# Kernel tuning notes

Measured on AMD Instinct MI355X. Metric: run time of the kernel, lower is better.

Reference implementation:

```python
import jax, jax.numpy as jnp
import numpy as np

B, S, C, P, M, H = 64, 512, 862, 96, 512, 128  # batch, seq_len, enc_in, pred_len, mem_num, hid_size


def setup_inputs() -> dict:
    key = jax.random.key(0)
    ks = jax.random.split(key, 8)
    x = jax.random.normal(ks[0], (B, S, C), dtype=jnp.float32)
    # nn.Linear default init scale ~ 1/sqrt(fan_in)
    W1 = jax.random.normal(ks[1], (H, S), dtype=jnp.float32) / np.float32(np.sqrt(S))
    b1 = jnp.zeros((H,), dtype=jnp.float32)
    Wp = jax.random.normal(ks[2], (H, H), dtype=jnp.float32) / np.float32(np.sqrt(H))
    bp = jnp.zeros((H,), dtype=jnp.float32)
    W2 = jax.random.normal(ks[3], (P, 2 * H), dtype=jnp.float32) / np.float32(np.sqrt(2 * H))
    b2 = jnp.zeros((P,), dtype=jnp.float32)
    # xavier_normal_ with relu gain: std = sqrt(2) * sqrt(2/(fan_in+fan_out))
    mem_std = np.float32(np.sqrt(2.0) * np.sqrt(2.0 / (M + H)))
    memory = jax.random.normal(ks[4], (M, H), dtype=jnp.float32) * mem_std
    return dict(x=x, W1=W1, b1=b1, Wp=Wp, bp=bp, W2=W2, b2=b2, memory=memory)


def reference(x, W1, b1, Wp, bp, W2, b2, memory):
    b, s, c = x.shape
    # get_repre: Linear1 over seq dim, sigmoid, projector
    r = jax.nn.sigmoid(jnp.einsum('bsc,hs->bch', x, W1) + b1)   # [B, C, H]
    r = jnp.einsum('bch,gh->bcg', r, Wp) + bp                    # [B, C, H]
    r = r.reshape(-1, H)                                         # [N, H], N = B*C
    # memory_enhance: codebook attention (topk/distance loss does not affect output)
    att = jax.nn.softmax(jnp.einsum('nd,fd->nf', r, memory), axis=1)  # [N, M]
    out = jnp.einsum('nf,fd->nd', att, memory)                        # [N, H]
    rep = jnp.concatenate([out, r], axis=1).reshape(b, c, 2 * H)      # [B, C, 2H]
    # predict: Linear2 then permute to [B, pred_len, C]
    res = jnp.einsum('bcd,pd->bcp', rep, W2) + b2
    return jnp.transpose(res, (0, 2, 1))
```

## Files before the change

### kernel.cpp

```cpp
#include <hip/hip_runtime.h>
#include <hip/hip_bf16.h>

typedef __attribute__((ext_vector_type(4))) float f32x4;
typedef __attribute__((ext_vector_type(8))) short s16x8;

#define DEVI __device__ __forceinline__

constexpr int S = 512, C = 862, P = 96, H = 128, BATCH = 64;

DEVI short f2bf(float f) {
  unsigned u = __builtin_bit_cast(unsigned, f);
  u += 0x7fffu + ((u >> 16) & 1u);
  return (short)(u >> 16);
}

DEVI unsigned pk2(float a, float b) {
  return (unsigned)(unsigned short)f2bf(a) | ((unsigned)(unsigned short)f2bf(b) << 16);
}

DEVI s16x8 mk8(const float* v) {
  s16x8 r;
#pragma unroll
  for (int i = 0; i < 8; ++i) r[i] = f2bf(v[i]);
  return r;
}

DEVI void gload16(const void* g, void* l) {
  __builtin_amdgcn_global_load_lds(
      (const __attribute__((address_space(1))) void*)g,
      (__attribute__((address_space(3))) void*)l, 16, 0, 0);
}

template <int NK>
DEVI void redistN(const unsigned* p01, const unsigned* p23, int sA, int hi,
                  s16x8* f) {
#pragma unroll
  for (int kc = 0; kc < NK; ++kc) {
    unsigned a0 = __shfl(p01[2 * kc], sA),      b0 = __shfl(p01[2 * kc + 1], sA);
    unsigned a1 = __shfl(p23[2 * kc], sA),      b1 = __shfl(p23[2 * kc + 1], sA);
    unsigned a2 = __shfl(p01[2 * kc], sA + 16), b2 = __shfl(p01[2 * kc + 1], sA + 16);
    unsigned a3 = __shfl(p23[2 * kc], sA + 16), b3 = __shfl(p23[2 * kc + 1], sA + 16);
    union { s16x8 v; unsigned u[4]; } t;
    t.u[0] = hi ? b0 : a0;
    t.u[1] = hi ? b1 : a1;
    t.u[2] = hi ? b2 : a2;
    t.u[3] = hi ? b3 : a3;
    f[kc] = t.v;
  }
}

__global__ __launch_bounds__(256) void k0_convert(
    const float* __restrict__ W1, const float* __restrict__ Wp,
    const float* __restrict__ W2, const float* __restrict__ mem,
    short* __restrict__ W1b, short* __restrict__ WpS, short* __restrict__ W2b,
    short* __restrict__ membS, short* __restrict__ memTS) {
  int i = blockIdx.x * 256 + threadIdx.x;
  if (i < 65536) { W1b[i] = f2bf(W1[i]); return; }
  i -= 65536;
  if (i < 16384) {
    int g = i >> 7, h = i & 127;
    WpS[(g << 7) + (h ^ ((g & 7) << 3))] = f2bf(Wp[i]);
    return;
  }
  i -= 16384;
  if (i < 24576) { W2b[i] = f2bf(W2[i]); return; }
  i -= 24576;
  if (i < 65536) {
    int f = i >> 7, d = i & 127;
    short v = f2bf(mem[i]);
    membS[((f >> 6) << 13) + ((f & 63) << 7) + (d ^ ((f & 7) << 3))] = v;
    memTS[((f >> 6) << 13) + (d << 6) + ((f & 63) ^ ((d & 7) << 3))] = v;
  }
}

__global__ __launch_bounds__(512, 2) void k12_fused(
    const float* __restrict__ x, const short* __restrict__ W1b,
    const float* __restrict__ b1, const short* __restrict__ WpS,
    const float* __restrict__ bp, const short* __restrict__ membS,
    const short* __restrict__ memTS, const short* __restrict__ W2b,
    const float* __restrict__ b2, float* __restrict__ out) {
  __shared__ __align__(16) char lds[49664];
  float* resf = (float*)lds;

  const int b = blockIdx.y, c0 = blockIdx.x * 128;
  const int valid = (C - c0 < 128) ? (C - c0) : 128;
  const int tid = threadIdx.x, l = tid & 63, w = tid >> 6;
  const int l15 = l & 15, l4 = l >> 4;
  const int sA = l15 + 32 * (l4 & 1);
  const int hi = (l4 >> 1) & 1;
  const int xr = (l15 & 7) << 4;
  const int cb = l4 * 16;
  const int rloc = 16 * w + l15;

  s16x8 rb[4];
  {
    short* xt = (short*)lds;
    short* w1t = (short*)(lds + 16384);
    const int cme = tid & 127, o2 = tid >> 7;
    const bool cv = (c0 + cme) < C;
    const float* xsrc0 = x + (size_t)b * S * C + c0 + cme;
    const int hh = tid >> 2, qq = tid & 3;

    f32x4 acc[8];
#pragma unroll
    for (int t = 0; t < 8; ++t) acc[t] = (f32x4){0.f, 0.f, 0.f, 0.f};

    float xv[2][8];
    s16x8 wv[2];
    {
#pragma unroll
      for (int j = 0; j < 2; ++j) {
        const float* src = xsrc0 + (size_t)((o2 + j * 4) * 8) * C;
#pragma unroll
        for (int i = 0; i < 8; ++i) xv[j][i] = cv ? src[(size_t)i * C] : 0.f;
      }
      const short* wsrc = W1b + hh * 512;
      wv[0] = *(const s16x8*)&wsrc[qq * 8];
      wv[1] = *(const s16x8*)&wsrc[(qq + 4) * 8];
    }

    for (int kt = 0; kt < 8; ++kt) {
#pragma unroll
      for (int j = 0; j < 2; ++j)
        *(s16x8*)&xt[cme * 64 + ((o2 + j * 4) ^ (cme & 7)) * 8] = mk8(xv[j]);
      *(s16x8*)&w1t[hh * 64 + (qq ^ (hh & 7)) * 8] = wv[0];
      *(s16x8*)&w1t[hh * 64 + ((qq + 4) ^ (hh & 7)) * 8] = wv[1];
      if (kt < 7) {
        int kn = kt + 1;
#pragma unroll
        for (int j = 0; j < 2; ++j) {
          const float* src = xsrc0 + (size_t)(kn * 64 + (o2 + j * 4) * 8) * C;
#pragma unroll
          for (int i = 0; i < 8; ++i) xv[j][i] = cv ? src[(size_t)i * C] : 0.f;
        }
        const short* wsrc = W1b + hh * 512 + kn * 64;
        wv[0] = *(const s16x8*)&wsrc[qq * 8];
        wv[1] = *(const s16x8*)&wsrc[(qq + 4) * 8];
      }
      __syncthreads();
      s16x8 bx[2];
#pragma unroll
      for (int kc = 0; kc < 2; ++kc)
        bx[kc] = *(const s16x8*)&xt[rloc * 64 + ((kc * 4 + l4) ^ (l15 & 7)) * 8];
#pragma unroll
      for (int t = 0; t < 8; ++t) {
#pragma unroll
        for (int kc = 0; kc < 2; ++kc) {
          s16x8 af = *(const s16x8*)&w1t[(t * 16 + l15) * 64 + ((kc * 4 + l4) ^ (l15 & 7)) * 8];
          acc[t] = __builtin_amdgcn_mfma_f32_16x16x32_bf16(af, bx[kc], acc[t], 0, 0, 0);
        }
      }
      __syncthreads();
    }

    {
      const char* gwp = (const char*)WpS;
      const char* gmb = (const char*)membS;
#pragma unroll
      for (int i = 0; i < 4; ++i) {
        int o = (w * 4 + i) * 1024;
        gload16(gwp + o + l * 16, lds + 16384 + o);
      }
#pragma unroll
      for (int i = 0; i < 2; ++i) {
        int o = (w * 2 + i) * 1024;
        gload16(gmb + o + l * 16, lds + o);
      }
    }

    unsigned p01[8], p23[8];
#pragma unroll
    for (int t = 0; t < 8; ++t) {
      f32x4 bq = *(const f32x4*)&b1[t * 16 + l4 * 4];
      float s0 = 1.f / (1.f + __expf(-(acc[t][0] + bq[0])));
      float s1 = 1.f / (1.f + __expf(-(acc[t][1] + bq[1])));
      float s2 = 1.f / (1.f + __expf(-(acc[t][2] + bq[2])));
      float s3 = 1.f / (1.f + __expf(-(acc[t][3] + bq[3])));
      p01[t] = pk2(s0, s1);
      p23[t] = pk2(s2, s3);
    }
    redistN<4>(p01, p23, sA, hi, rb);
  }
  __syncthreads();

  unsigned rpk01[8], rpk23[8];
  {
    const char* bufWp = lds + 16384;
#pragma unroll
    for (int gt = 0; gt < 8; ++gt) {
      f32x4 acc = (f32x4){0.f, 0.f, 0.f, 0.f};
#pragma unroll
      for (int kc = 0; kc < 4; ++kc) {
        s16x8 af = *(const s16x8*)(bufWp + (gt * 16 + l15) * 256 + ((kc * 64 + cb) ^ xr));
        acc = __builtin_amdgcn_mfma_f32_16x16x32_bf16(af, rb[kc], acc, 0, 0, 0);
      }
      f32x4 bq = *(const f32x4*)&bp[gt * 16 + l4 * 4];
      rpk01[gt] = pk2(acc[0] + bq[0], acc[1] + bq[1]);
      rpk23[gt] = pk2(acc[2] + bq[2], acc[3] + bq[3]);
    }
  }
  s16x8 r2f[4];
  redistN<4>(rpk01, rpk23, sA, hi, r2f);

  float m_run = -1e30f, s_run = 0.f;
  f32x4 oacc[8];
#pragma unroll
  for (int dt = 0; dt < 8; ++dt) oacc[dt] = (f32x4){0.f, 0.f, 0.f, 0.f};

  for (int s5 = 0; s5 < 8; ++s5) {
    __syncthreads();
    {
      const char* gmt = (const char*)memTS + (size_t)s5 * 16384;
#pragma unroll
      for (int i = 0; i < 2; ++i) {
        int o = (w * 2 + i) * 1024;
        gload16(gmt + o + l * 16, lds + 32768 + o);
      }
    }
    if (s5 < 7) {
      const char* gmb = (const char*)membS + (size_t)(s5 + 1) * 16384;
#pragma unroll
      for (int i = 0; i < 2; ++i) {
        int o = (w * 2 + i) * 1024;
        gload16(gmb + o + l * 16, lds + (((s5 + 1) & 1) << 14) + o);
      }
    }
    f32x4 lg[4];
    {
      const char* bmb = lds + ((s5 & 1) << 14);
#pragma unroll
      for (int ft = 0; ft < 4; ++ft) {
        lg[ft] = (f32x4){0.f, 0.f, 0.f, 0.f};
#pragma unroll
        for (int kc = 0; kc < 4; ++kc) {
          s16x8 af = *(const s16x8*)(bmb + (ft * 16 + l15) * 256 + ((kc * 64 + cb) ^ xr));
          lg[ft] = __builtin_amdgcn_mfma_f32_16x16x32_bf16(af, r2f[kc], lg[ft], 0, 0, 0);
        }
      }
    }
    s16x8 pf[2];
    {
      float mx = lg[0][0];
#pragma unroll
      for (int ft = 0; ft < 4; ++ft)
#pragma unroll
        for (int e = 0; e < 4; ++e) mx = fmaxf(mx, lg[ft][e]);
      mx = fmaxf(mx, __shfl_xor(mx, 16));
      mx = fmaxf(mx, __shfl_xor(mx, 32));
      if (s5 == 0) {
        m_run = mx;
      } else if (!__all(mx <= m_run + 8.f)) {
        float mn = fmaxf(m_run, mx);
        float sc = __expf(m_run - mn);
        s_run *= sc;
        m_run = mn;
#pragma unroll
        for (int dt = 0; dt < 8; ++dt)
#pragma unroll
          for (int e = 0; e < 4; ++e) oacc[dt][e] *= sc;
      }
      float ps = 0.f;
      unsigned ppk01[4], ppk23[4];
#pragma unroll
      for (int ft = 0; ft < 4; ++ft) {
#pragma unroll
        for (int e = 0; e < 4; ++e) {
          float p = __expf(lg[ft][e] - m_run);
          lg[ft][e] = p;
          ps += p;
        }
        ppk01[ft] = pk2(lg[ft][0], lg[ft][1]);
        ppk23[ft] = pk2(lg[ft][2], lg[ft][3]);
      }
      ps += __shfl_xor(ps, 16);
      ps += __shfl_xor(ps, 32);
      s_run += ps;
      redistN<2>(ppk01, ppk23, sA, hi, pf);
    }
    __syncthreads();
    {
      const char* bmt = lds + 32768;
#pragma unroll
      for (int dt = 0; dt < 8; ++dt) {
#pragma unroll
        for (int kc = 0; kc < 2; ++kc) {
          s16x8 af = *(const s16x8*)(bmt + (dt * 16 + l15) * 128 + ((kc * 64 + cb) ^ xr));
          oacc[dt] = __builtin_amdgcn_mfma_f32_16x16x32_bf16(af, pf[kc], oacc[dt], 0, 0, 0);
        }
      }
    }
  }
  __syncthreads();

  s16x8 of[4];
  {
    float inv = 1.f / s_run;
    unsigned opk01[8], opk23[8];
#pragma unroll
    for (int dt = 0; dt < 8; ++dt) {
      opk01[dt] = pk2(oacc[dt][0] * inv, oacc[dt][1] * inv);
      opk23[dt] = pk2(oacc[dt][2] * inv, oacc[dt][3] * inv);
    }
    redistN<4>(opk01, opk23, sA, hi, of);
  }

#pragma unroll
  for (int pt = 0; pt < 6; ++pt) {
    f32x4 acc = (f32x4){0.f, 0.f, 0.f, 0.f};
#pragma unroll
    for (int kc = 0; kc < 4; ++kc) {
      s16x8 af = *(const s16x8*)&W2b[(pt * 16 + l15) * 256 + kc * 32 + l4 * 8];
      acc = __builtin_amdgcn_mfma_f32_16x16x32_bf16(af, of[kc], acc, 0, 0, 0);
    }
#pragma unroll
    for (int kc = 0; kc < 4; ++kc) {
      s16x8 af = *(const s16x8*)&W2b[(pt * 16 + l15) * 256 + 128 + kc * 32 + l4 * 8];
      acc = __builtin_amdgcn_mfma_f32_16x16x32_bf16(af, r2f[kc], acc, 0, 0, 0);
    }
    f32x4 bq = *(const f32x4*)&b2[pt * 16 + l4 * 4];
#pragma unroll
    for (int e = 0; e < 4; ++e)
      resf[rloc * 97 + pt * 16 + l4 * 4 + e] = acc[e] + bq[e];
  }
  __syncthreads();
  {
    int c = tid & 127, p0 = tid >> 7;
    if (c < valid) {
      float* dst = out + (size_t)b * P * C + c0 + c;
#pragma unroll
      for (int j = 0; j < 24; ++j) {
        int p = p0 + j * 4;
        dst[(size_t)p * C] = resf[c * 97 + p];
      }
    }
  }
}

extern "C" void kernel_launch(void* const* d_in, const int* in_sizes, int n_in,
                              void* d_out, int out_size, void* d_ws, size_t ws_size,
                              hipStream_t stream) {
  const float* x   = (const float*)d_in[0];
  const float* W1  = (const float*)d_in[1];
  const float* b1  = (const float*)d_in[2];
  const float* Wp  = (const float*)d_in[3];
  const float* bpv = (const float*)d_in[4];
  const float* W2  = (const float*)d_in[5];
  const float* b2  = (const float*)d_in[6];
  const float* mem = (const float*)d_in[7];
  char* ws = (char*)d_ws;
  short* W1b   = (short*)(ws);
  short* WpS   = (short*)(ws + 131072);
  short* W2b   = (short*)(ws + 163840);
  short* membS = (short*)(ws + 212992);
  short* memTS = (short*)(ws + 344064);
  float* outp = (float*)d_out;

  k0_convert<<<672, 256, 0, stream>>>(W1, Wp, W2, mem, W1b, WpS, W2b, membS, memTS);
  dim3 grid(7, BATCH);
  k12_fused<<<grid, 512, 0, stream>>>(x, W1b, b1, WpS, bpv, membS, memTS, W2b, b2, outp);
}
```

Before: 82.33 us.

## Double block to 1024 threads, split memory attention across two warp groups with merge

The fused kernel now launches 1024 threads per block and divides the work into two groups of 8 waves. In stage 1 the two groups split the H output tiles of the W1 GEMM and exchange the sigmoid results through LDS. In the attention stage each group handles half of the 512 codebook entries with its own online softmax, and the two partial results are merged through LDS using the running max and sum. The change aims to raise parallelism and latency hiding per block. In exchange it adds more LDS (64KB), extra barriers, a bf16-rounded merge of partial outputs, and leaves half the waves idle during the final W2 projection. Launch bounds of (1024,2) with 64KB LDS may also limit occupancy or register budget.

```diff
diff --git a/kernel.cpp b/kernel.cpp
--- a/kernel.cpp
+++ b/kernel.cpp
@@ -17,6 +17,9 @@
 DEVI unsigned pk2(float a, float b) {
   return (unsigned)(unsigned short)f2bf(a) | ((unsigned)(unsigned short)f2bf(b) << 16);
 }
+
+DEVI float bflo(unsigned u) { return __builtin_bit_cast(float, u << 16); }
+DEVI float bfhi(unsigned u) { return __builtin_bit_cast(float, u & 0xffff0000u); }
 
 DEVI s16x8 mk8(const float* v) {
   s16x8 r;
@@ -68,74 +71,68 @@
   if (i < 65536) {
     int f = i >> 7, d = i & 127;
     short v = f2bf(mem[i]);
-    membS[((f >> 6) << 13) + ((f & 63) << 7) + (d ^ ((f & 7) << 3))] = v;
-    memTS[((f >> 6) << 13) + (d << 6) + ((f & 63) ^ ((d & 7) << 3))] = v;
-  }
-}
-
-__global__ __launch_bounds__(512, 2) void k12_fused(
+    membS[((f >> 5) << 12) + ((f & 31) << 7) + (d ^ ((f & 7) << 3))] = v;
+    int fo = (f >> 3) & 3, sw = (d ^ (d >> 2)) & 3;
+    memTS[((f >> 5) << 12) + (d << 5) + ((fo ^ sw) << 3) + (f & 7)] = v;
+  }
+}
+
+__global__ __launch_bounds__(1024, 2) void k12_fused(
     const float* __restrict__ x, const short* __restrict__ W1b,
     const float* __restrict__ b1, const short* __restrict__ WpS,
     const float* __restrict__ bp, const short* __restrict__ membS,
     const short* __restrict__ memTS, const short* __restrict__ W2b,
     const float* __restrict__ b2, float* __restrict__ out) {
-  __shared__ __align__(16) char lds[49664];
+  __shared__ __align__(16) char lds[65536];
   float* resf = (float*)lds;
 
   const int b = blockIdx.y, c0 = blockIdx.x * 128;
   const int valid = (C - c0 < 128) ? (C - c0) : 128;
   const int tid = threadIdx.x, l = tid & 63, w = tid >> 6;
+  const int g = w >> 3, wl = w & 7;
   const int l15 = l & 15, l4 = l >> 4;
   const int sA = l15 + 32 * (l4 & 1);
   const int hi = (l4 >> 1) & 1;
   const int xr = (l15 & 7) << 4;
   const int cb = l4 * 16;
-  const int rloc = 16 * w + l15;
+  const int rloc = 16 * wl + l15;
 
   s16x8 rb[4];
   {
     short* xt = (short*)lds;
     short* w1t = (short*)(lds + 16384);
-    const int cme = tid & 127, o2 = tid >> 7;
+    const int cme = tid & 127, oct = tid >> 7;
     const bool cv = (c0 + cme) < C;
     const float* xsrc0 = x + (size_t)b * S * C + c0 + cme;
-    const int hh = tid >> 2, qq = tid & 3;
-
-    f32x4 acc[8];
-#pragma unroll
-    for (int t = 0; t < 8; ++t) acc[t] = (f32x4){0.f, 0.f, 0.f, 0.f};
-
-    float xv[2][8];
-    s16x8 wv[2];
-    {
-#pragma unroll
-      for (int j = 0; j < 2; ++j) {
-        const float* src = xsrc0 + (size_t)((o2 + j * 4) * 8) * C;
-#pragma unroll
-        for (int i = 0; i < 8; ++i) xv[j][i] = cv ? src[(size_t)i * C] : 0.f;
-      }
-      const short* wsrc = W1b + hh * 512;
-      wv[0] = *(const s16x8*)&wsrc[qq * 8];
-      wv[1] = *(const s16x8*)&wsrc[(qq + 4) * 8];
+    const int hh = tid >> 3, qq = tid & 7;
+
+    {
+      const char* gwp = (const char*)WpS;
+      gload16(gwp + w * 2048 + l * 16, lds + 32768 + w * 2048);
+      gload16(gwp + w * 2048 + 1024 + l * 16, lds + 32768 + w * 2048 + 1024);
+    }
+
+    f32x4 acc[4];
+#pragma unroll
+    for (int t = 0; t < 4; ++t) acc[t] = (f32x4){0.f, 0.f, 0.f, 0.f};
+
+    float xv[8];
+    s16x8 wv;
+    {
+      const float* src = xsrc0 + (size_t)(oct * 8) * C;
+#pragma unroll
+      for (int i = 0; i < 8; ++i) xv[i] = cv ? src[(size_t)i * C] : 0.f;
+      wv = *(const s16x8*)&W1b[hh * 512 + qq * 8];
     }
 
     for (int kt = 0; kt < 8; ++kt) {
-#pragma unroll
-      for (int j = 0; j < 2; ++j)
-        *(s16x8*)&xt[cme * 64 + ((o2 + j * 4) ^ (cme & 7)) * 8] = mk8(xv[j]);
-      *(s16x8*)&w1t[hh * 64 + (qq ^ (hh & 7)) * 8] = wv[0];
-      *(s16x8*)&w1t[hh * 64 + ((qq + 4) ^ (hh & 7)) * 8] = wv[1];
+      *(s16x8*)&xt[cme * 64 + (oct ^ (cme & 7)) * 8] = mk8(xv);
+      *(s16x8*)&w1t[hh * 64 + (qq ^ (hh & 7)) * 8] = wv;
       if (kt < 7) {
-        int kn = kt + 1;
-#pragma unroll
-        for (int j = 0; j < 2; ++j) {
-          const float* src = xsrc0 + (size_t)(kn * 64 + (o2 + j * 4) * 8) * C;
-#pragma unroll
-          for (int i = 0; i < 8; ++i) xv[j][i] = cv ? src[(size_t)i * C] : 0.f;
-        }
-        const short* wsrc = W1b + hh * 512 + kn * 64;
-        wv[0] = *(const s16x8*)&wsrc[qq * 8];
-        wv[1] = *(const s16x8*)&wsrc[(qq + 4) * 8];
+        const float* src = xsrc0 + (size_t)((kt + 1) * 64 + oct * 8) * C;
+#pragma unroll
+        for (int i = 0; i < 8; ++i) xv[i] = cv ? src[(size_t)i * C] : 0.f;
+        wv = *(const s16x8*)&W1b[hh * 512 + (kt + 1) * 64 + qq * 8];
       }
       __syncthreads();
       s16x8 bx[2];
@@ -143,49 +140,42 @@
       for (int kc = 0; kc < 2; ++kc)
         bx[kc] = *(const s16x8*)&xt[rloc * 64 + ((kc * 4 + l4) ^ (l15 & 7)) * 8];
 #pragma unroll
-      for (int t = 0; t < 8; ++t) {
+      for (int t = 0; t < 4; ++t) {
+        int tg = 4 * g + t;
 #pragma unroll
         for (int kc = 0; kc < 2; ++kc) {
-          s16x8 af = *(const s16x8*)&w1t[(t * 16 + l15) * 64 + ((kc * 4 + l4) ^ (l15 & 7)) * 8];
+          s16x8 af = *(const s16x8*)&w1t[(tg * 16 + l15) * 64 + ((kc * 4 + l4) ^ (l15 & 7)) * 8];
           acc[t] = __builtin_amdgcn_mfma_f32_16x16x32_bf16(af, bx[kc], acc[t], 0, 0, 0);
         }
       }
       __syncthreads();
     }
 
-    {
-      const char* gwp = (const char*)WpS;
-      const char* gmb = (const char*)membS;
-#pragma unroll
-      for (int i = 0; i < 4; ++i) {
-        int o = (w * 4 + i) * 1024;
-        gload16(gwp + o + l * 16, lds + 16384 + o);
-      }
-#pragma unroll
-      for (int i = 0; i < 2; ++i) {
-        int o = (w * 2 + i) * 1024;
-        gload16(gmb + o + l * 16, lds + o);
-      }
-    }
-
-    unsigned p01[8], p23[8];
-#pragma unroll
-    for (int t = 0; t < 8; ++t) {
-      f32x4 bq = *(const f32x4*)&b1[t * 16 + l4 * 4];
+    short* r1ex = (short*)lds;
+#pragma unroll
+    for (int t = 0; t < 4; ++t) {
+      int tg = 4 * g + t;
+      f32x4 bq = *(const f32x4*)&b1[tg * 16 + l4 * 4];
       float s0 = 1.f / (1.f + __expf(-(acc[t][0] + bq[0])));
       float s1 = 1.f / (1.f + __expf(-(acc[t][1] + bq[1])));
       float s2 = 1.f / (1.f + __expf(-(acc[t][2] + bq[2])));
       float s3 = 1.f / (1.f + __expf(-(acc[t][3] + bq[3])));
-      p01[t] = pk2(s0, s1);
-      p23[t] = pk2(s2, s3);
-    }
-    redistN<4>(p01, p23, sA, hi, rb);
-  }
-  __syncthreads();
+      int slot = tg * 2 + (l4 >> 1);
+      int ahw = rloc * 128 + ((slot ^ (rloc & 7)) << 3) + (l4 & 1) * 4;
+      uint2 pp;
+      pp.x = pk2(s0, s1);
+      pp.y = pk2(s2, s3);
+      *(uint2*)&r1ex[ahw] = pp;
+    }
+    __syncthreads();
+#pragma unroll
+    for (int kc = 0; kc < 4; ++kc)
+      rb[kc] = *(const s16x8*)&r1ex[rloc * 128 + ((kc * 4 + l4) ^ (rloc & 7)) * 8];
+  }
 
   unsigned rpk01[8], rpk23[8];
   {
-    const char* bufWp = lds + 16384;
+    const char* bufWp = lds + 32768;
 #pragma unroll
     for (int gt = 0; gt < 8; ++gt) {
       f32x4 acc = (f32x4){0.f, 0.f, 0.f, 0.f};
@@ -201,35 +191,34 @@
   }
   s16x8 r2f[4];
   redistN<4>(rpk01, rpk23, sA, hi, r2f);
+  __syncthreads();
+
+  {
+    const char* gmb = (const char*)membS + (size_t)(g * 8) * 8192;
+    gload16(gmb + wl * 1024 + l * 16, lds + g * 16384 + wl * 1024);
+  }
 
   float m_run = -1e30f, s_run = 0.f;
   f32x4 oacc[8];
 #pragma unroll
   for (int dt = 0; dt < 8; ++dt) oacc[dt] = (f32x4){0.f, 0.f, 0.f, 0.f};
 
-  for (int s5 = 0; s5 < 8; ++s5) {
+  for (int j = 0; j < 8; ++j) {
     __syncthreads();
     {
-      const char* gmt = (const char*)memTS + (size_t)s5 * 16384;
-#pragma unroll
-      for (int i = 0; i < 2; ++i) {
-        int o = (w * 2 + i) * 1024;
-        gload16(gmt + o + l * 16, lds + 32768 + o);
-      }
-    }
-    if (s5 < 7) {
-      const char* gmb = (const char*)membS + (size_t)(s5 + 1) * 16384;
-#pragma unroll
-      for (int i = 0; i < 2; ++i) {
-        int o = (w * 2 + i) * 1024;
-        gload16(gmb + o + l * 16, lds + (((s5 + 1) & 1) << 14) + o);
-      }
-    }
-    f32x4 lg[4];
-    {
-      const char* bmb = lds + ((s5 & 1) << 14);
-#pragma unroll
-      for (int ft = 0; ft < 4; ++ft) {
+      const char* gmt = (const char*)memTS + (size_t)(g * 8 + j) * 8192;
+      gload16(gmt + wl * 1024 + l * 16, lds + 32768 + g * 8192 + wl * 1024);
+    }
+    if (j < 7) {
+      const char* gmb = (const char*)membS + (size_t)(g * 8 + j + 1) * 8192;
+      gload16(gmb + wl * 1024 + l * 16,
+              lds + g * 16384 + ((j + 1) & 1) * 8192 + wl * 1024);
+    }
+    f32x4 lg[2];
+    {
+      const char* bmb = lds + g * 16384 + (j & 1) * 8192;
+#pragma unroll
+      for (int ft = 0; ft < 2; ++ft) {
         lg[ft] = (f32x4){0.f, 0.f, 0.f, 0.f};
 #pragma unroll
         for (int kc = 0; kc < 4; ++kc) {
@@ -238,16 +227,16 @@
         }
       }
     }
-    s16x8 pf[2];
+    s16x8 pf[1];
     {
       float mx = lg[0][0];
 #pragma unroll
-      for (int ft = 0; ft < 4; ++ft)
+      for (int ft = 0; ft < 2; ++ft)
 #pragma unroll
         for (int e = 0; e < 4; ++e) mx = fmaxf(mx, lg[ft][e]);
       mx = fmaxf(mx, __shfl_xor(mx, 16));
       mx = fmaxf(mx, __shfl_xor(mx, 32));
-      if (s5 == 0) {
+      if (j == 0) {
         m_run = mx;
       } else if (!__all(mx <= m_run + 8.f)) {
         float mn = fmaxf(m_run, mx);
@@ -260,9 +249,9 @@
           for (int e = 0; e < 4; ++e) oacc[dt][e] *= sc;
       }
       float ps = 0.f;
-      unsigned ppk01[4], ppk23[4];
-#pragma unroll
-      for (int ft = 0; ft < 4; ++ft) {
+      unsigned ppk01[2], ppk23[2];
+#pragma unroll
+      for (int ft = 0; ft < 2; ++ft) {
 #pragma unroll
         for (int e = 0; e < 4; ++e) {
           float p = __expf(lg[ft][e] - m_run);
@@ -275,52 +264,84 @@
       ps += __shfl_xor(ps, 16);
       ps += __shfl_xor(ps, 32);
       s_run += ps;
-      redistN<2>(ppk01, ppk23, sA, hi, pf);
+      redistN<1>(ppk01, ppk23, sA, hi, pf);
     }
     __syncthreads();
     {
-      const char* bmt = lds + 32768;
+      const char* bmt = lds + 32768 + g * 8192;
 #pragma unroll
       for (int dt = 0; dt < 8; ++dt) {
-#pragma unroll
-        for (int kc = 0; kc < 2; ++kc) {
-          s16x8 af = *(const s16x8*)(bmt + (dt * 16 + l15) * 128 + ((kc * 64 + cb) ^ xr));
-          oacc[dt] = __builtin_amdgcn_mfma_f32_16x16x32_bf16(af, pf[kc], oacc[dt], 0, 0, 0);
-        }
-      }
-    }
-  }
-  __syncthreads();
-
+        int row = dt * 16 + l15;
+        s16x8 af = *(const s16x8*)(bmt + row * 64 + ((l4 ^ ((row ^ (row >> 2)) & 3)) << 4));
+        oacc[dt] = __builtin_amdgcn_mfma_f32_16x16x32_bf16(af, pf[0], oacc[dt], 0, 0, 0);
+      }
+    }
+  }
+
+  float* mz = (float*)(lds + 49152);
+  float* sz = (float*)(lds + 50176);
+  if (l4 == 0) {
+    mz[g * 128 + rloc] = m_run;
+    sz[g * 128 + rloc] = s_run;
+  }
+  __syncthreads();
+  float mO = mz[(1 - g) * 128 + rloc];
+  float sO = sz[(1 - g) * 128 + rloc];
+  float m = fmaxf(m_run, mO);
+  float sclS = __expf(m_run - m);
+  float s_tot = s_run * sclS + sO * __expf(mO - m);
+  short* mrg = (short*)lds;
+  if (g == 1) {
+#pragma unroll
+    for (int dt = 0; dt < 8; ++dt) {
+      int slot = dt * 2 + (l4 >> 1);
+      int ahw = rloc * 128 + ((slot ^ (rloc & 15)) << 3) + (l4 & 1) * 4;
+      uint2 pp;
+      pp.x = pk2(oacc[dt][0] * sclS, oacc[dt][1] * sclS);
+      pp.y = pk2(oacc[dt][2] * sclS, oacc[dt][3] * sclS);
+      *(uint2*)&mrg[ahw] = pp;
+    }
+  }
+  __syncthreads();
   s16x8 of[4];
-  {
-    float inv = 1.f / s_run;
+  if (g == 0) {
+    float inv = 1.f / s_tot;
     unsigned opk01[8], opk23[8];
 #pragma unroll
     for (int dt = 0; dt < 8; ++dt) {
-      opk01[dt] = pk2(oacc[dt][0] * inv, oacc[dt][1] * inv);
-      opk23[dt] = pk2(oacc[dt][2] * inv, oacc[dt][3] * inv);
+      int slot = dt * 2 + (l4 >> 1);
+      int ahw = rloc * 128 + ((slot ^ (rloc & 15)) << 3) + (l4 & 1) * 4;
+      uint2 pp = *(const uint2*)&mrg[ahw];
+      float o0 = (oacc[dt][0] * sclS + bflo(pp.x)) * inv;
+      float o1 = (oacc[dt][1] * sclS + bfhi(pp.x)) * inv;
+      float o2 = (oacc[dt][2] * sclS + bflo(pp.y)) * inv;
+      float o3 = (oacc[dt][3] * sclS + bfhi(pp.y)) * inv;
+      opk01[dt] = pk2(o0, o1);
+      opk23[dt] = pk2(o2, o3);
     }
     redistN<4>(opk01, opk23, sA, hi, of);
   }
-
-#pragma unroll
-  for (int pt = 0; pt < 6; ++pt) {
-    f32x4 acc = (f32x4){0.f, 0.f, 0.f, 0.f};
-#pragma unroll
-    for (int kc = 0; kc < 4; ++kc) {
-      s16x8 af = *(const s16x8*)&W2b[(pt * 16 + l15) * 256 + kc * 32 + l4 * 8];
-      acc = __builtin_amdgcn_mfma_f32_16x16x32_bf16(af, of[kc], acc, 0, 0, 0);
-    }
-#pragma unroll
-    for (int kc = 0; kc < 4; ++kc) {
-      s16x8 af = *(const s16x8*)&W2b[(pt * 16 + l15) * 256 + 128 + kc * 32 + l4 * 8];
-      acc = __builtin_amdgcn_mfma_f32_16x16x32_bf16(af, r2f[kc], acc, 0, 0, 0);
-    }
-    f32x4 bq = *(const f32x4*)&b2[pt * 16 + l4 * 4];
-#pragma unroll
-    for (int e = 0; e < 4; ++e)
-      resf[rloc * 97 + pt * 16 + l4 * 4 + e] = acc[e] + bq[e];
+  __syncthreads();
+
+  if (g == 0) {
+#pragma unroll
+    for (int pt = 0; pt < 6; ++pt) {
+      f32x4 acc = (f32x4){0.f, 0.f, 0.f, 0.f};
+#pragma unroll
+      for (int kc = 0; kc < 4; ++kc) {
+        s16x8 af = *(const s16x8*)&W2b[(pt * 16 + l15) * 256 + kc * 32 + l4 * 8];
+        acc = __builtin_amdgcn_mfma_f32_16x16x32_bf16(af, of[kc], acc, 0, 0, 0);
+      }
+#pragma unroll
+      for (int kc = 0; kc < 4; ++kc) {
+        s16x8 af = *(const s16x8*)&W2b[(pt * 16 + l15) * 256 + 128 + kc * 32 + l4 * 8];
+        acc = __builtin_amdgcn_mfma_f32_16x16x32_bf16(af, r2f[kc], acc, 0, 0, 0);
+      }
+      f32x4 bq = *(const f32x4*)&b2[pt * 16 + l4 * 4];
+#pragma unroll
+      for (int e = 0; e < 4; ++e)
+        resf[rloc * 97 + pt * 16 + l4 * 4 + e] = acc[e] + bq[e];
+    }
   }
   __syncthreads();
   {
@@ -328,8 +349,8 @@
     if (c < valid) {
       float* dst = out + (size_t)b * P * C + c0 + c;
 #pragma unroll
-      for (int j = 0; j < 24; ++j) {
-        int p = p0 + j * 4;
+      for (int j = 0; j < 12; ++j) {
+        int p = p0 + j * 8;
         dst[(size_t)p * C] = resf[c * 97 + p];
       }
     }
@@ -357,5 +378,5 @@
 
   k0_convert<<<672, 256, 0, stream>>>(W1, Wp, W2, mem, W1b, WpS, W2b, membS, memTS);
   dim3 grid(7, BATCH);
-  k12_fused<<<grid, 512, 0, stream>>>(x, W1b, b1, WpS, bpv, membS, memTS, W2b, b2, outp);
-}
+  k12_fused<<<grid, 1024, 0, stream>>>(x, W1b, b1, WpS, bpv, membS, memTS, W2b, b2, outp);
+}
```

New measurement: 105.0 us. 1.28x slower.

## Double K-tile and memory chunk sizes, halving loop trips and barriers

Applied to the files above, without the earlier changes.

The first GEMM's K tile grows from 64 to 128 and the memory attention loop processes 128 codebook rows per step instead of 64. Both loops therefore run half as many iterations with half as many barriers. The LDS layout is reorganized with a 16-way XOR swizzle, and the memory buffers are repacked to match. The membS prefetch is now issued after the second barrier, so it overlaps the PV MFMAs instead of being double-buffered. In exchange, LDS grows to 64KB and register pressure rises (xv[4][8], lg[8]), which may reduce occupancy below 2 blocks per CU.

```diff
diff --git a/kernel.cpp b/kernel.cpp
--- a/kernel.cpp
+++ b/kernel.cpp
@@ -68,8 +68,9 @@
   if (i < 65536) {
     int f = i >> 7, d = i & 127;
     short v = f2bf(mem[i]);
-    membS[((f >> 6) << 13) + ((f & 63) << 7) + (d ^ ((f & 7) << 3))] = v;
-    memTS[((f >> 6) << 13) + (d << 6) + ((f & 63) ^ ((d & 7) << 3))] = v;
+    int row = f & 127, sl = f >> 7;
+    membS[sl * 16384 + row * 128 + (((d >> 3) ^ (row & 15)) << 3) + (d & 7)] = v;
+    memTS[sl * 16384 + d * 128 + (((row >> 3) ^ (d & 15)) << 3) + (f & 7)] = v;
   }
 }
 
@@ -79,7 +80,7 @@
     const float* __restrict__ bp, const short* __restrict__ membS,
     const short* __restrict__ memTS, const short* __restrict__ W2b,
     const float* __restrict__ b2, float* __restrict__ out) {
-  __shared__ __align__(16) char lds[49664];
+  __shared__ __align__(16) char lds[65536];
   float* resf = (float*)lds;
 
   const int b = blockIdx.y, c0 = blockIdx.x * 128;
@@ -88,65 +89,66 @@
   const int l15 = l & 15, l4 = l >> 4;
   const int sA = l15 + 32 * (l4 & 1);
   const int hi = (l4 >> 1) & 1;
-  const int xr = (l15 & 7) << 4;
+  const int xr8 = (l15 & 7) << 4;
   const int cb = l4 * 16;
   const int rloc = 16 * w + l15;
 
   s16x8 rb[4];
   {
     short* xt = (short*)lds;
-    short* w1t = (short*)(lds + 16384);
+    short* w1t = (short*)(lds + 32768);
     const int cme = tid & 127, o2 = tid >> 7;
     const bool cv = (c0 + cme) < C;
     const float* xsrc0 = x + (size_t)b * S * C + c0 + cme;
-    const int hh = tid >> 2, qq = tid & 3;
+    const int hh = tid >> 2, qq4 = tid & 3;
 
     f32x4 acc[8];
 #pragma unroll
     for (int t = 0; t < 8; ++t) acc[t] = (f32x4){0.f, 0.f, 0.f, 0.f};
 
-    float xv[2][8];
-    s16x8 wv[2];
-    {
-#pragma unroll
-      for (int j = 0; j < 2; ++j) {
+    float xv[4][8];
+    s16x8 wv[4];
+    {
+#pragma unroll
+      for (int j = 0; j < 4; ++j) {
         const float* src = xsrc0 + (size_t)((o2 + j * 4) * 8) * C;
 #pragma unroll
         for (int i = 0; i < 8; ++i) xv[j][i] = cv ? src[(size_t)i * C] : 0.f;
       }
       const short* wsrc = W1b + hh * 512;
-      wv[0] = *(const s16x8*)&wsrc[qq * 8];
-      wv[1] = *(const s16x8*)&wsrc[(qq + 4) * 8];
-    }
-
-    for (int kt = 0; kt < 8; ++kt) {
-#pragma unroll
-      for (int j = 0; j < 2; ++j)
-        *(s16x8*)&xt[cme * 64 + ((o2 + j * 4) ^ (cme & 7)) * 8] = mk8(xv[j]);
-      *(s16x8*)&w1t[hh * 64 + (qq ^ (hh & 7)) * 8] = wv[0];
-      *(s16x8*)&w1t[hh * 64 + ((qq + 4) ^ (hh & 7)) * 8] = wv[1];
-      if (kt < 7) {
+#pragma unroll
+      for (int j = 0; j < 4; ++j) wv[j] = *(const s16x8*)&wsrc[(qq4 + j * 4) * 8];
+    }
+
+    for (int kt = 0; kt < 4; ++kt) {
+#pragma unroll
+      for (int j = 0; j < 4; ++j)
+        *(s16x8*)&xt[cme * 128 + ((o2 + j * 4) ^ (cme & 15)) * 8] = mk8(xv[j]);
+#pragma unroll
+      for (int j = 0; j < 4; ++j)
+        *(s16x8*)&w1t[hh * 128 + ((qq4 + j * 4) ^ (hh & 15)) * 8] = wv[j];
+      if (kt < 3) {
         int kn = kt + 1;
 #pragma unroll
-        for (int j = 0; j < 2; ++j) {
-          const float* src = xsrc0 + (size_t)(kn * 64 + (o2 + j * 4) * 8) * C;
+        for (int j = 0; j < 4; ++j) {
+          const float* src = xsrc0 + (size_t)(kn * 128 + (o2 + j * 4) * 8) * C;
 #pragma unroll
           for (int i = 0; i < 8; ++i) xv[j][i] = cv ? src[(size_t)i * C] : 0.f;
         }
-        const short* wsrc = W1b + hh * 512 + kn * 64;
-        wv[0] = *(const s16x8*)&wsrc[qq * 8];
-        wv[1] = *(const s16x8*)&wsrc[(qq + 4) * 8];
+        const short* wsrc = W1b + hh * 512 + kn * 128;
+#pragma unroll
+        for (int j = 0; j < 4; ++j) wv[j] = *(const s16x8*)&wsrc[(qq4 + j * 4) * 8];
       }
       __syncthreads();
-      s16x8 bx[2];
-#pragma unroll
-      for (int kc = 0; kc < 2; ++kc)
-        bx[kc] = *(const s16x8*)&xt[rloc * 64 + ((kc * 4 + l4) ^ (l15 & 7)) * 8];
+      s16x8 bx[4];
+#pragma unroll
+      for (int kc = 0; kc < 4; ++kc)
+        bx[kc] = *(const s16x8*)((char*)xt + rloc * 256 + (((kc * 4 + l4) ^ l15) << 4));
 #pragma unroll
       for (int t = 0; t < 8; ++t) {
 #pragma unroll
-        for (int kc = 0; kc < 2; ++kc) {
-          s16x8 af = *(const s16x8*)&w1t[(t * 16 + l15) * 64 + ((kc * 4 + l4) ^ (l15 & 7)) * 8];
+        for (int kc = 0; kc < 4; ++kc) {
+          s16x8 af = *(const s16x8*)((char*)w1t + (t * 16 + l15) * 256 + (((kc * 4 + l4) ^ l15) << 4));
           acc[t] = __builtin_amdgcn_mfma_f32_16x16x32_bf16(af, bx[kc], acc[t], 0, 0, 0);
         }
       }
@@ -159,12 +161,8 @@
 #pragma unroll
       for (int i = 0; i < 4; ++i) {
         int o = (w * 4 + i) * 1024;
-        gload16(gwp + o + l * 16, lds + 16384 + o);
-      }
-#pragma unroll
-      for (int i = 0; i < 2; ++i) {
-        int o = (w * 2 + i) * 1024;
-        gload16(gmb + o + l * 16, lds + o);
+        gload16(gwp + o + l * 16, lds + o);
+        gload16(gmb + o + l * 16, lds + 32768 + o);
       }
     }
 
@@ -185,13 +183,13 @@
 
   unsigned rpk01[8], rpk23[8];
   {
-    const char* bufWp = lds + 16384;
+    const char* bufWp = lds;
 #pragma unroll
     for (int gt = 0; gt < 8; ++gt) {
       f32x4 acc = (f32x4){0.f, 0.f, 0.f, 0.f};
 #pragma unroll
       for (int kc = 0; kc < 4; ++kc) {
-        s16x8 af = *(const s16x8*)(bufWp + (gt * 16 + l15) * 256 + ((kc * 64 + cb) ^ xr));
+        s16x8 af = *(const s16x8*)(bufWp + (gt * 16 + l15) * 256 + ((kc * 64 + cb) ^ xr8));
         acc = __builtin_amdgcn_mfma_f32_16x16x32_bf16(af, rb[kc], acc, 0, 0, 0);
       }
       f32x4 bq = *(const f32x4*)&bp[gt * 16 + l4 * 4];
@@ -207,42 +205,34 @@
 #pragma unroll
   for (int dt = 0; dt < 8; ++dt) oacc[dt] = (f32x4){0.f, 0.f, 0.f, 0.f};
 
-  for (int s5 = 0; s5 < 8; ++s5) {
+  for (int s5 = 0; s5 < 4; ++s5) {
     __syncthreads();
     {
-      const char* gmt = (const char*)memTS + (size_t)s5 * 16384;
-#pragma unroll
-      for (int i = 0; i < 2; ++i) {
-        int o = (w * 2 + i) * 1024;
-        gload16(gmt + o + l * 16, lds + 32768 + o);
-      }
-    }
-    if (s5 < 7) {
-      const char* gmb = (const char*)membS + (size_t)(s5 + 1) * 16384;
-#pragma unroll
-      for (int i = 0; i < 2; ++i) {
-        int o = (w * 2 + i) * 1024;
-        gload16(gmb + o + l * 16, lds + (((s5 + 1) & 1) << 14) + o);
-      }
-    }
-    f32x4 lg[4];
-    {
-      const char* bmb = lds + ((s5 & 1) << 14);
-#pragma unroll
-      for (int ft = 0; ft < 4; ++ft) {
+      const char* gmt = (const char*)memTS + (size_t)s5 * 32768;
+#pragma unroll
+      for (int i = 0; i < 4; ++i) {
+        int o = (w * 4 + i) * 1024;
+        gload16(gmt + o + l * 16, lds + o);
+      }
+    }
+    f32x4 lg[8];
+    {
+      const char* bmb = lds + 32768;
+#pragma unroll
+      for (int ft = 0; ft < 8; ++ft) {
         lg[ft] = (f32x4){0.f, 0.f, 0.f, 0.f};
 #pragma unroll
         for (int kc = 0; kc < 4; ++kc) {
-          s16x8 af = *(const s16x8*)(bmb + (ft * 16 + l15) * 256 + ((kc * 64 + cb) ^ xr));
+          s16x8 af = *(const s16x8*)(bmb + (ft * 16 + l15) * 256 + (((kc * 4 + l4) ^ l15) << 4));
           lg[ft] = __builtin_amdgcn_mfma_f32_16x16x32_bf16(af, r2f[kc], lg[ft], 0, 0, 0);
         }
       }
     }
-    s16x8 pf[2];
+    s16x8 pf[4];
     {
       float mx = lg[0][0];
 #pragma unroll
-      for (int ft = 0; ft < 4; ++ft)
+      for (int ft = 0; ft < 8; ++ft)
 #pragma unroll
         for (int e = 0; e < 4; ++e) mx = fmaxf(mx, lg[ft][e]);
       mx = fmaxf(mx, __shfl_xor(mx, 16));
@@ -260,9 +250,9 @@
           for (int e = 0; e < 4; ++e) oacc[dt][e] *= sc;
       }
       float ps = 0.f;
-      unsigned ppk01[4], ppk23[4];
-#pragma unroll
-      for (int ft = 0; ft < 4; ++ft) {
+      unsigned ppk01[8], ppk23[8];
+#pragma unroll
+      for (int ft = 0; ft < 8; ++ft) {
 #pragma unroll
         for (int e = 0; e < 4; ++e) {
           float p = __expf(lg[ft][e] - m_run);
@@ -275,16 +265,24 @@
       ps += __shfl_xor(ps, 16);
       ps += __shfl_xor(ps, 32);
       s_run += ps;
-      redistN<2>(ppk01, ppk23, sA, hi, pf);
+      redistN<4>(ppk01, ppk23, sA, hi, pf);
     }
     __syncthreads();
-    {
-      const char* bmt = lds + 32768;
+    if (s5 < 3) {
+      const char* gmb = (const char*)membS + (size_t)(s5 + 1) * 32768;
+#pragma unroll
+      for (int i = 0; i < 4; ++i) {
+        int o = (w * 4 + i) * 1024;
+        gload16(gmb + o + l * 16, lds + 32768 + o);
+      }
+    }
+    {
+      const char* bmt = lds;
 #pragma unroll
       for (int dt = 0; dt < 8; ++dt) {
 #pragma unroll
-        for (int kc = 0; kc < 2; ++kc) {
-          s16x8 af = *(const s16x8*)(bmt + (dt * 16 + l15) * 128 + ((kc * 64 + cb) ^ xr));
+        for (int kc = 0; kc < 4; ++kc) {
+          s16x8 af = *(const s16x8*)(bmt + (dt * 16 + l15) * 256 + (((kc * 4 + l4) ^ l15) << 4));
           oacc[dt] = __builtin_amdgcn_mfma_f32_16x16x32_bf16(af, pf[kc], oacc[dt], 0, 0, 0);
         }
       }
```

Result: slower. 95.89 us (+16.5%).
